# Performance work log

Measured on AMD Instinct MI355X. Metric: run time of the kernel, lower is better.

The kernel has to match this reference:

```python
import jax, jax.numpy as jnp
import numpy as np

NUM_LEVELS = 2
THETA = 0.5
EPS = 1e-5  # torch F.instance_norm default eps


def _patch_sigmoid_attn(x, p):
    # Non-overlapping patch instance-norm + sigmoid. For p==0 (n=1) this is a
    # full per-(B,C) instance norm, matching the original p==0 branch.
    B, C, H, W = x.shape
    n = 2 ** p                      # patches per spatial dim (kh==sh => fold is a reshape)
    sph, spw = H // n, W // n       # patch size
    xp = x.reshape(B, C, n, sph, n, spw)
    mu = xp.mean(axis=(3, 5), keepdims=True)
    var = xp.var(axis=(3, 5), keepdims=True)  # biased var, as in torch instance_norm
    w = jax.nn.sigmoid((xp - mu) * jax.lax.rsqrt(var + EPS))
    return w.reshape(B, C, H, W)


def setup_inputs() -> dict:
    key = jax.random.key(0)
    k1, _ = jax.random.split(key)
    x = jax.random.normal(k1, (8, 64, 256, 256), dtype=jnp.float32)
    level_weights = jnp.ones((NUM_LEVELS + 1,), dtype=jnp.float32) / (NUM_LEVELS + 1)
    return {"x": x, "level_weights": level_weights}


def reference(x, level_weights):
    feats = []
    for p in range(NUM_LEVELS, -1, -1):  # coarse-to-fine, p=0 last (order matters for weights)
        w = _patch_sigmoid_attn(x, p)
        feats.append(THETA * x + (1.0 - THETA) * w * x)
    lw = jax.nn.softmax(level_weights)
    out = lw[0] * feats[0]
    for i in range(1, NUM_LEVELS + 1):
        out = out + lw[i] * feats[i]
    return out
```

## Files before the change

kernel.cpp:

```cpp
#include <hip/hip_runtime.h>

#define EPS 1e-5f
#define LOG2E 1.4426950408889634f


__global__ __launch_bounds__(256) void k_stats(const float4* __restrict__ x4,
                                               float2* __restrict__ part) {
    const int P    = blockIdx.x;
    const int bc   = P >> 4;
    const int pidx = P & 15;
    const int pr   = pidx >> 2, pc = pidx & 3;
    const int t    = threadIdx.x;
    const long chan4 = (long)bc << 14;

    float s = 0.f, ss = 0.f;
#pragma unroll
    for (int k = 0; k < 4; ++k) {
        const int q    = k * 256 + t;
        const int row  = q >> 4;
        const int col4 = q & 15;
        const float4 v = x4[chan4 + (long)(pr * 64 + row) * 64 + pc * 16 + col4];
        s  += v.x + v.y + v.z + v.w;
        ss += v.x * v.x + v.y * v.y + v.z * v.z + v.w * v.w;
    }
#pragma unroll
    for (int off = 32; off > 0; off >>= 1) {
        s  += __shfl_down(s, off, 64);
        ss += __shfl_down(ss, off, 64);
    }
    __shared__ float2 red[4];
    const int wave = t >> 6, lane = t & 63;
    if (lane == 0) red[wave] = make_float2(s, ss);
    __syncthreads();
    if (t == 0) {
        float S = 0.f, SS = 0.f;
#pragma unroll
        for (int i = 0; i < 4; ++i) { S += red[i].x; SS += red[i].y; }
        part[P] = make_float2(S, SS);
    }
}

__global__ __launch_bounds__(64) void k_agg(const float2* __restrict__ part,
                                            const float* __restrict__ lw,
                                            float2* __restrict__ S,
                                            float* __restrict__ lws) {
    const int bc = blockIdx.x;
    const int t  = threadIdx.x;
    __shared__ float2 ps[16];
    if (t < 16) ps[t] = part[bc * 16 + t];
    __syncthreads();

    if (t < 21) {
        float sum = 0.f, sq = 0.f, n;
        if (t < 16) {
            sum = ps[t].x; sq = ps[t].y; n = 4096.f;
        } else if (t < 20) {
            const int g = t - 16, gr = g >> 1, gc = g & 1;
            const int b = 8 * gr + 2 * gc;
            sum = ps[b].x + ps[b + 1].x + ps[b + 4].x + ps[b + 5].x;
            sq  = ps[b].y + ps[b + 1].y + ps[b + 4].y + ps[b + 5].y;
            n = 16384.f;
        } else {
#pragma unroll
            for (int i = 0; i < 16; ++i) { sum += ps[i].x; sq += ps[i].y; }
            n = 65536.f;
        }
        const float mu   = sum / n;
        const float var  = sq / n - mu * mu;
        const float rstd = rsqrtf(var + EPS);
        S[bc * 21 + t] = make_float2(-rstd * LOG2E, mu * rstd * LOG2E);
    }
    if (bc == 0 && t == 21) {
        const float w0 = lw[0], w1 = lw[1], w2 = lw[2];
        const float mx = fmaxf(w0, fmaxf(w1, w2));
        const float e0 = __expf(w0 - mx), e1 = __expf(w1 - mx), e2 = __expf(w2 - mx);
        const float inv = 1.f / (e0 + e1 + e2);
        lws[0] = e0 * inv;
        lws[1] = e1 * inv;
        lws[2] = e2 * inv;
    }
}

__global__ __launch_bounds__(256) void k_apply(const float4* __restrict__ x4,
                                               const float2* __restrict__ S,
                                               const float* __restrict__ lws,
                                               float4* __restrict__ out4) {
    const long i = (long)blockIdx.x * 256 + threadIdx.x;
    const int bc = (int)(i >> 14);
    const int f  = (int)(i & 16383);
    const int h  = f >> 6;
    const int w4 = f & 63;

    const float lwA = lws[0], lwB = lws[1], lwC = lws[2];
    const float2* Sc = S + bc * 21;
    const float2 c2 = Sc[(h >> 6) * 4 + (w4 >> 4)];
    const float2 c1 = Sc[16 + (h >> 7) * 2 + (w4 >> 5)];
    const float2 c0 = Sc[20];

    const float4 v = x4[i];
    float4 r;
#define ELT(comp)                                                              \
    {                                                                          \
        const float xv = v.comp;                                               \
        const float e2 = __builtin_amdgcn_exp2f(fmaf(xv, c2.x, c2.y));         \
        const float e1 = __builtin_amdgcn_exp2f(fmaf(xv, c1.x, c1.y));         \
        const float e0 = __builtin_amdgcn_exp2f(fmaf(xv, c0.x, c0.y));         \
        const float pA = 1.f + e2, pB = 1.f + e1, pC = 1.f + e0;               \
        const float mBC = pB * pC, mAB = pA * pB, mAC = pA * pC;               \
        const float num = fmaf(lwA, mBC, fmaf(lwB, mAC, lwC * mAB));           \
        const float den = mAB * pC;                                            \
        const float t0  = 0.5f * xv;                                           \
        r.comp = fmaf(t0 * num, __builtin_amdgcn_rcpf(den), t0);               \
    }
    ELT(x) ELT(y) ELT(z) ELT(w)
#undef ELT
    out4[i] = r;
}

extern "C" void kernel_launch(void* const* d_in, const int* in_sizes, int n_in,
                              void* d_out, int out_size, void* d_ws, size_t ws_size,
                              hipStream_t stream) {
    const float* x  = (const float*)d_in[0];
    const float* lw = (const float*)d_in[1];
    float* out      = (float*)d_out;

    float2* part = (float2*)d_ws;
    float2* S    = part + 8192;
    float*  lws  = (float*)(S + 512 * 21);

    k_stats<<<8192, 256, 0, stream>>>((const float4*)x, part);
    k_agg<<<512, 64, 0, stream>>>(part, lw, S, lws);
    k_apply<<<32768, 256, 0, stream>>>((const float4*)x, S, lws, (float4*)out);
}
```

Measured before the change: 247.4 us.

## Fuse stats, aggregation and apply into one register-resident kernel per channel

Replaces the three-kernel pipeline (patch stats, aggregation, elementwise apply) with a single kernel that launches one 1024-thread block per (B,C) channel. Each wave loads one 64x64 patch into registers (16 float4 per thread), reduces it, and computes all 21 level coefficients in shared memory. It then applies the sigmoid blend from registers, so x is read from HBM once instead of twice and two extra launches go away. Loads and stores are nontemporal. The trade-offs are heavy register pressure (64 floats per thread at 1024 threads), only 512 blocks, and no overlap between the load and compute phases inside a block.

New measurement: 221.6 us, median of 2. -10.4%, faster.

```diff
diff --git a/kernel.cpp b/kernel.cpp
--- a/kernel.cpp
+++ b/kernel.cpp
@@ -3,51 +3,39 @@
 #define EPS 1e-5f
 #define LOG2E 1.4426950408889634f
 
+typedef float f32x4 __attribute__((ext_vector_type(4)));
 
-__global__ __launch_bounds__(256) void k_stats(const float4* __restrict__ x4,
-                                               float2* __restrict__ part) {
-    const int P    = blockIdx.x;
-    const int bc   = P >> 4;
-    const int pidx = P & 15;
-    const int pr   = pidx >> 2, pc = pidx & 3;
+__global__ __launch_bounds__(1024) void k_fused(const f32x4* __restrict__ x4,
+                                                const float* __restrict__ lw,
+                                                f32x4* __restrict__ out4) {
+    const int bc   = blockIdx.x;
     const int t    = threadIdx.x;
-    const long chan4 = (long)bc << 14;
+    const int w    = t >> 6, lane = t & 63;
+    const int pr   = w >> 2, pc = w & 3;
+    const int base = (bc << 14) + (pr * 64 + (lane >> 4)) * 64 + pc * 16 + (lane & 15);
+
+    f32x4 d[16];
+#pragma unroll
+    for (int it = 0; it < 16; ++it)
+        d[it] = __builtin_nontemporal_load(x4 + base + it * 256);
 
     float s = 0.f, ss = 0.f;
 #pragma unroll
-    for (int k = 0; k < 4; ++k) {
-        const int q    = k * 256 + t;
-        const int row  = q >> 4;
-        const int col4 = q & 15;
-        const float4 v = x4[chan4 + (long)(pr * 64 + row) * 64 + pc * 16 + col4];
-        s  += v.x + v.y + v.z + v.w;
-        ss += v.x * v.x + v.y * v.y + v.z * v.z + v.w * v.w;
+    for (int it = 0; it < 16; ++it) {
+        const f32x4 v = d[it];
+        s  += v[0] + v[1] + v[2] + v[3];
+        ss += v[0] * v[0] + v[1] * v[1] + v[2] * v[2] + v[3] * v[3];
     }
 #pragma unroll
     for (int off = 32; off > 0; off >>= 1) {
         s  += __shfl_down(s, off, 64);
         ss += __shfl_down(ss, off, 64);
     }
-    __shared__ float2 red[4];
-    const int wave = t >> 6, lane = t & 63;
-    if (lane == 0) red[wave] = make_float2(s, ss);
-    __syncthreads();
-    if (t == 0) {
-        float S = 0.f, SS = 0.f;
-#pragma unroll
-        for (int i = 0; i < 4; ++i) { S += red[i].x; SS += red[i].y; }
-        part[P] = make_float2(S, SS);
-    }
-}
 
-__global__ __launch_bounds__(64) void k_agg(const float2* __restrict__ part,
-                                            const float* __restrict__ lw,
-                                            float2* __restrict__ S,
-                                            float* __restrict__ lws) {
-    const int bc = blockIdx.x;
-    const int t  = threadIdx.x;
     __shared__ float2 ps[16];
-    if (t < 16) ps[t] = part[bc * 16 + t];
+    __shared__ float2 coefs[21];
+    __shared__ float  lws[3];
+    if (lane == 0) ps[w] = make_float2(s, ss);
     __syncthreads();
 
     if (t < 21) {
@@ -68,53 +56,43 @@
         const float mu   = sum / n;
         const float var  = sq / n - mu * mu;
         const float rstd = rsqrtf(var + EPS);
-        S[bc * 21 + t] = make_float2(-rstd * LOG2E, mu * rstd * LOG2E);
+        coefs[t] = make_float2(-rstd * LOG2E, mu * rstd * LOG2E);
     }
-    if (bc == 0 && t == 21) {
+    if (t == 21) {
         const float w0 = lw[0], w1 = lw[1], w2 = lw[2];
         const float mx = fmaxf(w0, fmaxf(w1, w2));
-        const float e0 = __expf(w0 - mx), e1 = __expf(w1 - mx), e2 = __expf(w2 - mx);
-        const float inv = 1.f / (e0 + e1 + e2);
-        lws[0] = e0 * inv;
-        lws[1] = e1 * inv;
-        lws[2] = e2 * inv;
+        const float a0 = __expf(w0 - mx), a1 = __expf(w1 - mx), a2 = __expf(w2 - mx);
+        const float inv = 1.f / (a0 + a1 + a2);
+        lws[0] = a0 * inv;
+        lws[1] = a1 * inv;
+        lws[2] = a2 * inv;
     }
-}
+    __syncthreads();
 
-__global__ __launch_bounds__(256) void k_apply(const float4* __restrict__ x4,
-                                               const float2* __restrict__ S,
-                                               const float* __restrict__ lws,
-                                               float4* __restrict__ out4) {
-    const long i = (long)blockIdx.x * 256 + threadIdx.x;
-    const int bc = (int)(i >> 14);
-    const int f  = (int)(i & 16383);
-    const int h  = f >> 6;
-    const int w4 = f & 63;
+    const float2 c2 = coefs[w];
+    const float2 c1 = coefs[16 + (pr >> 1) * 2 + (pc >> 1)];
+    const float2 c0 = coefs[20];
+    const float lwA = lws[0], lwB = lws[1], lwC = lws[2];
 
-    const float lwA = lws[0], lwB = lws[1], lwC = lws[2];
-    const float2* Sc = S + bc * 21;
-    const float2 c2 = Sc[(h >> 6) * 4 + (w4 >> 4)];
-    const float2 c1 = Sc[16 + (h >> 7) * 2 + (w4 >> 5)];
-    const float2 c0 = Sc[20];
-
-    const float4 v = x4[i];
-    float4 r;
-#define ELT(comp)                                                              \
-    {                                                                          \
-        const float xv = v.comp;                                               \
-        const float e2 = __builtin_amdgcn_exp2f(fmaf(xv, c2.x, c2.y));         \
-        const float e1 = __builtin_amdgcn_exp2f(fmaf(xv, c1.x, c1.y));         \
-        const float e0 = __builtin_amdgcn_exp2f(fmaf(xv, c0.x, c0.y));         \
-        const float pA = 1.f + e2, pB = 1.f + e1, pC = 1.f + e0;               \
-        const float mBC = pB * pC, mAB = pA * pB, mAC = pA * pC;               \
-        const float num = fmaf(lwA, mBC, fmaf(lwB, mAC, lwC * mAB));           \
-        const float den = mAB * pC;                                            \
-        const float t0  = 0.5f * xv;                                           \
-        r.comp = fmaf(t0 * num, __builtin_amdgcn_rcpf(den), t0);               \
+#pragma unroll
+    for (int it = 0; it < 16; ++it) {
+        const f32x4 v = d[it];
+        f32x4 r;
+#pragma unroll
+        for (int j = 0; j < 4; ++j) {
+            const float xv = v[j];
+            const float e2 = __builtin_amdgcn_exp2f(fmaf(xv, c2.x, c2.y));
+            const float e1 = __builtin_amdgcn_exp2f(fmaf(xv, c1.x, c1.y));
+            const float e0 = __builtin_amdgcn_exp2f(fmaf(xv, c0.x, c0.y));
+            const float pA = 1.f + e2, pB = 1.f + e1, pC = 1.f + e0;
+            const float mBC = pB * pC, mAB = pA * pB, mAC = pA * pC;
+            const float num = fmaf(lwA, mBC, fmaf(lwB, mAC, lwC * mAB));
+            const float den = mAB * pC;
+            const float t0  = 0.5f * xv;
+            r[j] = fmaf(t0 * num, __builtin_amdgcn_rcpf(den), t0);
+        }
+        __builtin_nontemporal_store(r, out4 + base + it * 256);
     }
-    ELT(x) ELT(y) ELT(z) ELT(w)
-#undef ELT
-    out4[i] = r;
 }
 
 extern "C" void kernel_launch(void* const* d_in, const int* in_sizes, int n_in,
@@ -123,12 +101,7 @@
     const float* x  = (const float*)d_in[0];
     const float* lw = (const float*)d_in[1];
     float* out      = (float*)d_out;
+    (void)d_ws; (void)ws_size;
 
-    float2* part = (float2*)d_ws;
-    float2* S    = part + 8192;
-    float*  lws  = (float*)(S + 512 * 21);
-
-    k_stats<<<8192, 256, 0, stream>>>((const float4*)x, part);
-    k_agg<<<512, 64, 0, stream>>>(part, lw, S, lws);
-    k_apply<<<32768, 256, 0, stream>>>((const float4*)x, S, lws, (float4*)out);
+    k_fused<<<512, 1024, 0, stream>>>((const f32x4*)x, lw, (f32x4*)out);
 }
```
